# Kernel tuning notes

Hardware: AMD Instinct MI355X
Metric: run time of the kernel (lower is better)

The kernel has to match this reference:

```python
import jax, jax.numpy as jnp
import numpy as np

B, N = 2, 2048
D_MODEL, HEADS = 512, 8
D_K = D_MODEL // HEADS
D_HIDDEN = 2048
MIN_SPREAD = 2.0
MIN_RBF = 1e-3
MAX_RBF = 1.0
LN_EPS = 1e-5


def setup_inputs() -> dict:
    key = jax.random.key(0)
    ks = jax.random.split(key, 12)
    xs = (6.0 / (D_K + D_MODEL)) ** 0.5
    q = jax.random.normal(ks[0], (B, N, D_MODEL), dtype=jnp.float32)
    k = jax.random.normal(ks[1], (B, N, D_MODEL), dtype=jnp.float32)
    v = jax.random.normal(ks[2], (B, N, D_MODEL), dtype=jnp.float32)
    coords = jax.random.normal(ks[3], (B, N, 3), dtype=jnp.float32) * 10.0
    mask = jnp.ones((B, N), dtype=bool)
    q_proj = jax.random.uniform(ks[4], (HEADS, D_MODEL, D_K), minval=-xs, maxval=xs)
    k_proj = jax.random.uniform(ks[5], (HEADS, D_MODEL, D_K), minval=-xs, maxval=xs)
    v_proj = jax.random.uniform(ks[6], (HEADS, D_MODEL, D_K), minval=-xs, maxval=xs)
    q_bias = jnp.zeros((HEADS, D_K))
    k_bias = jnp.zeros((HEADS, D_K))
    v_bias = jnp.zeros((HEADS, D_K))
    ow = (1.0 / D_MODEL) ** 0.5
    out_w = jax.random.uniform(ks[7], (D_MODEL, D_MODEL), minval=-ow, maxval=ow)
    spread_w = jnp.zeros((HEADS,))
    beta_w = jnp.zeros((HEADS,))
    ln1_g = jnp.ones((D_MODEL,)); ln1_b = jnp.zeros((D_MODEL,))
    ln2_g = jnp.ones((D_MODEL,)); ln2_b = jnp.zeros((D_MODEL,))
    w1 = jax.random.normal(ks[8], (D_MODEL, D_HIDDEN)) * 0.02
    b1 = jnp.zeros((D_HIDDEN,))
    w2 = jax.random.normal(ks[9], (D_HIDDEN, D_MODEL)) * 0.02
    b2 = jnp.zeros((D_MODEL,))
    return dict(q=q, k=k, v=v, coords=coords, mask=mask,
                q_proj=q_proj, k_proj=k_proj, v_proj=v_proj,
                q_bias=q_bias, k_bias=k_bias, v_bias=v_bias,
                out_w=out_w, spread_w=spread_w, beta_w=beta_w,
                ln1_g=ln1_g, ln1_b=ln1_b, ln2_g=ln2_g, ln2_b=ln2_b,
                w1=w1, b1=b1, w2=w2, b2=b2)


def _layernorm(x, g, b):
    mu = jnp.mean(x, axis=-1, keepdims=True)
    var = jnp.mean((x - mu) ** 2, axis=-1, keepdims=True)
    return (x - mu) * jax.lax.rsqrt(var + LN_EPS) * g + b


def _geo_attention(q, k, v, coords, mask,
                   q_proj, k_proj, v_proj, q_bias, k_bias, v_bias,
                   out_w, spread_w, beta_w):
    # per-head projections: [B,H,N,dk]
    Q = jnp.einsum('bnd,hdk->bhnk', q, q_proj) + q_bias[None, :, None, :]
    K = jnp.einsum('bnd,hdk->bhnk', k, k_proj) + k_bias[None, :, None, :]
    V = jnp.einsum('bnd,hdk->bhnk', v, v_proj) + v_bias[None, :, None, :]

    spreads = MIN_SPREAD + jnp.exp(spread_w)   # [H]
    betas = jnp.exp(beta_w)                    # [H]

    # pairwise squared distances [B,N,N]
    d2 = jnp.sum((coords[:, :, None, :] - coords[:, None, :, :]) ** 2, axis=-1)
    # per-head Gaussian RBF [B,H,N,N]
    rbf = jnp.exp(-d2[:, None, :, :] / (2.0 * spreads[None, :, None, None] ** 2))

    scores = jnp.einsum('bhnk,bhmk->bhnm', Q, K) / jnp.sqrt(jnp.float32(D_K))
    scores = betas[None, :, None, None] * rbf * scores

    # sparsity: keys with rbf outside [min_rbf, max_rbf] or padded are masked out
    valid = (rbf >= MIN_RBF) & (rbf <= MAX_RBF) & mask[:, None, None, :]
    scores = jnp.where(valid, scores, -jnp.inf)
    attn = jax.nn.softmax(scores, axis=-1)     # diagonal always valid (rbf=1)

    out = jnp.einsum('bhnm,bhmk->bhnk', attn, V)         # [B,H,N,dk]
    # torch: out.permute(0,2,3,1).reshape(B,N,d_model) -> (b,n,dk,h) layout
    out = jnp.transpose(out, (0, 2, 3, 1)).reshape(out.shape[0], out.shape[2], D_MODEL)
    return out @ out_w.T


def reference(q, k, v, coords, mask,
              q_proj, k_proj, v_proj, q_bias, k_bias, v_bias,
              out_w, spread_w, beta_w,
              ln1_g, ln1_b, ln2_g, ln2_b, w1, b1, w2, b2):
    attn_out = _geo_attention(q, k, v, coords, mask,
                              q_proj, k_proj, v_proj, q_bias, k_bias, v_bias,
                              out_w, spread_w, beta_w)
    x = _layernorm(q + attn_out, ln1_g, ln1_b)
    ffn = jax.nn.relu(x @ w1 + b1) @ w2 + b2
    x = _layernorm(x + ffn, ln2_g, ln2_b)
    return x
```

## Files before the change

### kernel.cpp

```cpp
#include <hip/hip_runtime.h>
#include <math.h>

typedef __attribute__((ext_vector_type(8))) short bf16x8;
typedef __attribute__((ext_vector_type(4))) float f32x4;

#define MFMA16(a,b,c) __builtin_amdgcn_mfma_f32_16x16x32_bf16((a),(b),(c),0,0,0)

__device__ __forceinline__ unsigned short f2bf(float f) {
    union { float f; unsigned u; } x; x.f = f;
    unsigned r = x.u + 0x7FFFu + ((x.u >> 16) & 1u);
    return (unsigned short)(r >> 16);
}

__device__ __forceinline__ unsigned cvt_pk_bf16(float lo, float hi) {
    unsigned r;
    asm("v_cvt_pk_bf16_f32 %0, %1, %2" : "=v"(r) : "v"(lo), "v"(hi));
    return r;
}

__global__ __launch_bounds__(256) void cvt_qkv(
    const float* __restrict__ q, const float* __restrict__ k,
    const float* __restrict__ v,
    unsigned short* __restrict__ qb, unsigned short* __restrict__ kb,
    unsigned short* __restrict__ vb, int n)
{
    for (int i = blockIdx.x * 256 + threadIdx.x; i < n; i += gridDim.x * 256) {
        qb[i] = f2bf(q[i]); kb[i] = f2bf(k[i]); vb[i] = f2bf(v[i]);
    }
}

__global__ __launch_bounds__(256) void cvt_weights(
    const float* __restrict__ qp, const float* __restrict__ kp,
    const float* __restrict__ vp, const float* __restrict__ ow,
    const float* __restrict__ w1, const float* __restrict__ w2,
    unsigned short* __restrict__ qpT, unsigned short* __restrict__ kpT,
    unsigned short* __restrict__ vpT, unsigned short* __restrict__ owT,
    unsigned short* __restrict__ w1T, unsigned short* __restrict__ w2T)
{
    const int NP = 262144;
    const int total = 4 * NP + 1048576 + 1048576;
    for (int i = blockIdx.x * 256 + threadIdx.x; i < total; i += gridDim.x * 256) {
        if (i < 3 * NP) {
            int which = i / NP, r = i - which * NP;
            int n = r >> 9, d = r & 511;
            int h = n >> 6, kk = n & 63;
            const float* src = (which == 0) ? qp : (which == 1) ? kp : vp;
            unsigned short* dst = (which == 0) ? qpT : (which == 1) ? kpT : vpT;
            dst[r] = f2bf(src[(h << 15) + (d << 6) + kk]);
        } else if (i < 4 * NP) {
            int r = i - 3 * NP;
            int oi = r >> 9, f = r & 511;
            int h = f >> 6, kk = f & 63;
            owT[r] = f2bf(ow[(oi << 9) + (kk << 3) + h]);
        } else if (i < 4 * NP + 1048576) {
            int r = i - 4 * NP;
            int n = r >> 9, d = r & 511;
            w1T[r] = f2bf(w1[(d << 11) + n]);
        } else {
            int r = i - 4 * NP - 1048576;
            int n = r >> 11, d = r & 2047;
            w2T[r] = f2bf(w2[(d << 9) + n]);
        }
    }
}

template<int RELU, int SF32, int SB16, int SVTR>
__global__ __launch_bounds__(256) void gemm_bt(
    const unsigned short* __restrict__ A,
    const unsigned short* __restrict__ Bt,
    const float* __restrict__ bias,
    float* __restrict__ Cf, unsigned short* __restrict__ Cb,
    int M, int N, int K)
{
    __shared__ unsigned short As[128][72];
    __shared__ unsigned short Bs[128][72];
    const int tid = threadIdx.x;
    const int m0 = blockIdx.y << 7, n0 = blockIdx.x << 7;
    const int wv = tid >> 6, lane = tid & 63;
    const int lrow = lane & 15, kg = lane >> 4;
    const int wr = (wv >> 1) << 6, wc = (wv & 1) << 6;

    f32x4 acc[4][4];
    const f32x4 z4 = {0.f, 0.f, 0.f, 0.f};
#pragma unroll
    for (int i = 0; i < 4; ++i)
#pragma unroll
        for (int j = 0; j < 4; ++j) acc[i][j] = z4;

    const int nkt = K >> 6;
    for (int kt = 0; kt < nkt; ++kt) {
        __syncthreads();
        const int k0 = kt << 6;
#pragma unroll
        for (int i = 0; i < 4; ++i) {
            int slot = tid + (i << 8);
            int r = slot >> 3, c = (slot & 7) << 3;
            *(int4*)(&As[r][c]) = *(const int4*)(&A[(long)(m0 + r) * K + k0 + c]);
            *(int4*)(&Bs[r][c]) = *(const int4*)(&Bt[(long)(n0 + r) * K + k0 + c]);
        }
        __syncthreads();
#pragma unroll
        for (int ks = 0; ks < 2; ++ks) {
            const int koff = (ks << 5) + (kg << 3);
            bf16x8 af[4], bfr[4];
#pragma unroll
            for (int mi = 0; mi < 4; ++mi)
                af[mi] = *(const bf16x8*)(&As[wr + (mi << 4) + lrow][koff]);
#pragma unroll
            for (int ni = 0; ni < 4; ++ni)
                bfr[ni] = *(const bf16x8*)(&Bs[wc + (ni << 4) + lrow][koff]);
#pragma unroll
            for (int mi = 0; mi < 4; ++mi)
#pragma unroll
                for (int ni = 0; ni < 4; ++ni)
                    acc[mi][ni] = MFMA16(af[mi], bfr[ni], acc[mi][ni]);
        }
    }

#pragma unroll
    for (int mi = 0; mi < 4; ++mi) {
#pragma unroll
        for (int ni = 0; ni < 4; ++ni) {
            const int col = n0 + wc + (ni << 4) + lrow;
            const float bv = bias ? bias[col] : 0.0f;
#pragma unroll
            for (int j = 0; j < 4; ++j) {
                const int row = m0 + wr + (mi << 4) + (kg << 2) + j;
                float val = acc[mi][ni][j] + bv;
                if (RELU) val = fmaxf(val, 0.0f);
                if (SF32) Cf[(long)row * N + col] = val;
                if (SB16) Cb[(long)row * N + col] = f2bf(val);
                if (SVTR)
                    Cb[((long)(row >> 11) << 20) + ((long)col << 11) + (row & 2047)] = f2bf(val);
            }
        }
    }
}

__global__ __launch_bounds__(256) void geo_attn(
    const unsigned short* __restrict__ Qh,
    const unsigned short* __restrict__ Kh,
    const unsigned short* __restrict__ VhT,
    const float* __restrict__ coords,
    const float* __restrict__ spread_w, const float* __restrict__ beta_w,
    unsigned short* __restrict__ Ob)
{
    __shared__ unsigned short Qs[64][72];
    __shared__ unsigned short Ks[64][72];
    __shared__ unsigned short Vs[64][72];
    __shared__ unsigned short Ps[4][16][72];
    __shared__ float4 ck4[64];

    const int tid = threadIdx.x;
    const int bid = blockIdx.x;
    const int swz = ((bid & 7) << 6) + (bid >> 3);
    const int bh = swz >> 5, qt = swz & 31;
    const int b = bh >> 3, h = bh & 7;
    const int wv = tid >> 6, lane = tid & 63;
    const int lq = lane & 15, kg = lane >> 4;
    const float NEG_INF = -__builtin_inff();

    const float spread = 2.0f + __expf(spread_w[h]);
    const float inv2s2 = 1.0f / (2.0f * spread * spread);
    const float coef = __expf(beta_w[h]) * 0.125f;

    {
        const long qbase = ((long)(b * 2048 + qt * 64)) * 512 + h * 64;
#pragma unroll
        for (int i = 0; i < 2; ++i) {
            int slot = tid + (i << 8);
            int r = slot >> 3, c = (slot & 7) << 3;
            *(int4*)(&Qs[r][c]) = *(const int4*)(&Qh[qbase + (long)r * 512 + c]);
        }
    }

    float cqx, cqy, cqz;
    {
        long ca = ((long)(b * 2048 + qt * 64 + wv * 16 + lq)) * 3;
        cqx = coords[ca]; cqy = coords[ca + 1]; cqz = coords[ca + 2];
    }

    float mrun = NEG_INF, lrun = 0.0f;
    f32x4 Oa[4];
    const f32x4 z4 = {0.f, 0.f, 0.f, 0.f};
#pragma unroll
    for (int nd = 0; nd < 4; ++nd) Oa[nd] = z4;

    const long kbase0 = ((long)b * 2048) * 512 + h * 64;
    const long vbase = ((long)(b * 8 + h)) * 131072;

    for (int kt = 0; kt < 32; ++kt) {
        __syncthreads();
        const int k0 = kt << 6;
#pragma unroll
        for (int i = 0; i < 2; ++i) {
            int slot = tid + (i << 8);
            int r = slot >> 3, c = (slot & 7) << 3;
            *(int4*)(&Ks[r][c]) = *(const int4*)(&Kh[kbase0 + (long)(k0 + r) * 512 + c]);
            *(int4*)(&Vs[r][c]) = *(const int4*)(&VhT[vbase + (long)r * 2048 + k0 + c]);
        }
        if (tid < 64) {
            long ca = ((long)(b * 2048 + k0 + tid)) * 3;
            ck4[tid] = make_float4(coords[ca], coords[ca + 1], coords[ca + 2], 0.0f);
        }
        __syncthreads();

        f32x4 t4[4];
#pragma unroll
        for (int ra = 0; ra < 4; ++ra) t4[ra] = z4;
#pragma unroll
        for (int ks = 0; ks < 2; ++ks) {
            const int koff = (ks << 5) + (kg << 3);
            bf16x8 bq = *(const bf16x8*)(&Qs[(wv << 4) + lq][koff]);
#pragma unroll
            for (int ra = 0; ra < 4; ++ra) {
                bf16x8 ak = *(const bf16x8*)(&Ks[(ra << 4) + lq][koff]);
                t4[ra] = MFMA16(ak, bq, t4[ra]);
            }
        }

        float tmax = NEG_INF;
#pragma unroll
        for (int ra = 0; ra < 4; ++ra) {
#pragma unroll
            for (int j = 0; j < 4; ++j) {
                float4 ck = ck4[(ra << 4) + (kg << 2) + j];
                float dx = cqx - ck.x, dy = cqy - ck.y, dz = cqz - ck.z;
                float d2 = dx * dx + dy * dy + dz * dz;
                float rbf = __expf(-d2 * inv2s2);
                float val = (rbf >= 1e-3f) ? coef * rbf * t4[ra][j] : NEG_INF;
                t4[ra][j] = val;
                tmax = fmaxf(tmax, val);
            }
        }
        tmax = fmaxf(tmax, __shfl_xor(tmax, 16, 64));
        tmax = fmaxf(tmax, __shfl_xor(tmax, 32, 64));

        const float mn = fmaxf(mrun, tmax);
        const bool dead = (mn == NEG_INF);
        const float mneff = dead ? 0.0f : mn;
        const float fcorr = dead ? 1.0f : __expf(mrun - mn);

        float psum = 0.0f;
#pragma unroll
        for (int ra = 0; ra < 4; ++ra) {
#pragma unroll
            for (int j = 0; j < 4; ++j) {
                float p = __expf(t4[ra][j] - mneff);
                t4[ra][j] = p;
                psum += p;
            }
        }
        psum += __shfl_xor(psum, 16, 64);
        psum += __shfl_xor(psum, 32, 64);
        mrun = mn;
        lrun = lrun * fcorr + psum;

#pragma unroll
        for (int ra = 0; ra < 4; ++ra) {
            uint2 pk;
            pk.x = cvt_pk_bf16(t4[ra][0], t4[ra][1]);
            pk.y = cvt_pk_bf16(t4[ra][2], t4[ra][3]);
            *(uint2*)(&Ps[wv][lq][(ra << 4) + (kg << 2)]) = pk;
        }

        float fb[4];
#pragma unroll
        for (int j = 0; j < 4; ++j)
            fb[j] = __shfl(fcorr, (lane & 48) | ((kg << 2) + j), 64);
#pragma unroll
        for (int nd = 0; nd < 4; ++nd)
#pragma unroll
            for (int j = 0; j < 4; ++j)
                Oa[nd][j] *= fb[j];

#pragma unroll
        for (int ks = 0; ks < 2; ++ks) {
            const int koff = (ks << 5) + (kg << 3);
            bf16x8 ap = *(const bf16x8*)(&Ps[wv][lq][koff]);
#pragma unroll
            for (int nd = 0; nd < 4; ++nd) {
                bf16x8 bv = *(const bf16x8*)(&Vs[(nd << 4) + lq][koff]);
                Oa[nd] = MFMA16(ap, bv, Oa[nd]);
            }
        }
    }

    const float inv = 1.0f / lrun;
    float il[4];
#pragma unroll
    for (int j = 0; j < 4; ++j)
        il[j] = __shfl(inv, (lane & 48) | ((kg << 2) + j), 64);
    const long obase = ((long)(b * 2048 + qt * 64 + (wv << 4))) * 512 + h * 64;
#pragma unroll
    for (int nd = 0; nd < 4; ++nd)
#pragma unroll
        for (int j = 0; j < 4; ++j)
            Ob[obase + (long)((kg << 2) + j) * 512 + (nd << 4) + lq] =
                f2bf(Oa[nd][j] * il[j]);
}

template<int SB16>
__global__ __launch_bounds__(256) void ln_res(
    const float* __restrict__ X, const float* __restrict__ R,
    const float* __restrict__ g, const float* __restrict__ bb,
    float* __restrict__ Yf, unsigned short* __restrict__ Yb)
{
    const int wv = threadIdx.x >> 6, lane = threadIdx.x & 63;
    const long row = (long)blockIdx.x * 4 + wv;
    const float* xp = X + row * 512;
    const float* rp = R + row * 512;
    const int c0 = lane * 8;
    float4 a0 = *(const float4*)(xp + c0);
    float4 a1 = *(const float4*)(xp + c0 + 4);
    float4 r0 = *(const float4*)(rp + c0);
    float4 r1 = *(const float4*)(rp + c0 + 4);
    float v[8] = {a0.x + r0.x, a0.y + r0.y, a0.z + r0.z, a0.w + r0.w,
                  a1.x + r1.x, a1.y + r1.y, a1.z + r1.z, a1.w + r1.w};
    float s = 0.f, ss = 0.f;
#pragma unroll
    for (int i = 0; i < 8; ++i) { s += v[i]; ss += v[i] * v[i]; }
#pragma unroll
    for (int off = 1; off < 64; off <<= 1) {
        s += __shfl_xor(s, off, 64);
        ss += __shfl_xor(ss, off, 64);
    }
    const float mu = s * (1.0f / 512.0f);
    const float var = ss * (1.0f / 512.0f) - mu * mu;
    const float rstd = rsqrtf(var + 1e-5f);
#pragma unroll
    for (int i = 0; i < 8; ++i) {
        const int c = c0 + i;
        const float y = (v[i] - mu) * rstd * g[c] + bb[c];
        Yf[row * 512 + c] = y;
        if (SB16) Yb[row * 512 + c] = f2bf(y);
    }
}

extern "C" void kernel_launch(void* const* d_in, const int* in_sizes, int n_in,
                              void* d_out, int out_size, void* d_ws, size_t ws_size,
                              hipStream_t stream)
{
    const float* q      = (const float*)d_in[0];
    const float* k      = (const float*)d_in[1];
    const float* v      = (const float*)d_in[2];
    const float* coords = (const float*)d_in[3];
    const float* q_proj = (const float*)d_in[5];
    const float* k_proj = (const float*)d_in[6];
    const float* v_proj = (const float*)d_in[7];
    const float* q_bias = (const float*)d_in[8];
    const float* k_bias = (const float*)d_in[9];
    const float* v_bias = (const float*)d_in[10];
    const float* out_w  = (const float*)d_in[11];
    const float* spread_w = (const float*)d_in[12];
    const float* beta_w = (const float*)d_in[13];
    const float* ln1_g  = (const float*)d_in[14];
    const float* ln1_b  = (const float*)d_in[15];
    const float* ln2_g  = (const float*)d_in[16];
    const float* ln2_b  = (const float*)d_in[17];
    const float* w1     = (const float*)d_in[18];
    const float* b1     = (const float*)d_in[19];
    const float* w2     = (const float*)d_in[20];
    const float* b2     = (const float*)d_in[21];
    float* out = (float*)d_out;

    char* ws = (char*)d_ws;
    size_t off = 0;
    auto alloc = [&](size_t bytes) -> void* {
        void* p = ws + off;
        off += (bytes + 255) & ~(size_t)255;
        return p;
    };
    unsigned short* qb   = (unsigned short*)alloc(4096UL * 512 * 2);
    unsigned short* kb   = (unsigned short*)alloc(4096UL * 512 * 2);
    unsigned short* vb   = (unsigned short*)alloc(4096UL * 512 * 2);
    unsigned short* qpT  = (unsigned short*)alloc(512UL * 512 * 2);
    unsigned short* kpT  = (unsigned short*)alloc(512UL * 512 * 2);
    unsigned short* vpT  = (unsigned short*)alloc(512UL * 512 * 2);
    unsigned short* owT  = (unsigned short*)alloc(512UL * 512 * 2);
    unsigned short* w1T  = (unsigned short*)alloc(2048UL * 512 * 2);
    unsigned short* w2T  = (unsigned short*)alloc(512UL * 2048 * 2);
    unsigned short* Qp   = (unsigned short*)alloc(4096UL * 512 * 2);
    unsigned short* Kp   = (unsigned short*)alloc(4096UL * 512 * 2);
    unsigned short* VpT  = (unsigned short*)alloc(4096UL * 512 * 2);
    unsigned short* attnb= (unsigned short*)alloc(4096UL * 512 * 2);
    float* proj = (float*)alloc(4096UL * 512 * 4);
    float* x1   = (float*)alloc(4096UL * 512 * 4);
    unsigned short* x1b = (unsigned short*)alloc(4096UL * 512 * 2);
    unsigned short* hid = (unsigned short*)alloc(4096UL * 2048 * 2);
    float* ffn  = (float*)alloc(4096UL * 512 * 4);
    (void)ws_size; (void)in_sizes; (void)n_in; (void)out_size;

    cvt_qkv<<<2048, 256, 0, stream>>>(q, k, v, qb, kb, vb, 2097152);
    cvt_weights<<<2048, 256, 0, stream>>>(q_proj, k_proj, v_proj, out_w, w1, w2,
                                          qpT, kpT, vpT, owT, w1T, w2T);

    dim3 g512(4, 32);
    gemm_bt<0, 0, 1, 0><<<g512, 256, 0, stream>>>(qb, qpT, q_bias, nullptr, Qp, 4096, 512, 512);
    gemm_bt<0, 0, 1, 0><<<g512, 256, 0, stream>>>(kb, kpT, k_bias, nullptr, Kp, 4096, 512, 512);
    gemm_bt<0, 0, 0, 1><<<g512, 256, 0, stream>>>(vb, vpT, v_bias, nullptr, VpT, 4096, 512, 512);

    geo_attn<<<512, 256, 0, stream>>>(Qp, Kp, VpT, coords, spread_w, beta_w, attnb);

    gemm_bt<0, 1, 0, 0><<<g512, 256, 0, stream>>>(attnb, owT, nullptr, proj, nullptr, 4096, 512, 512);
    ln_res<1><<<1024, 256, 0, stream>>>(proj, q, ln1_g, ln1_b, x1, x1b);

    dim3 g2048(16, 32);
    gemm_bt<1, 0, 1, 0><<<g2048, 256, 0, stream>>>(x1b, w1T, b1, nullptr, hid, 4096, 2048, 512);
    gemm_bt<0, 1, 0, 0><<<g512, 256, 0, stream>>>(hid, w2T, b2, ffn, nullptr, 4096, 512, 2048);
    ln_res<0><<<1024, 256, 0, stream>>>(ffn, x1, ln2_g, ln2_b, out, nullptr);
}
```

Before: 229.6 us.

## Split attention keys across two blocks with register-prefetched tiles and merge kernel

After: 240.2 us. 1.05x slower.

```diff
diff --git a/kernel.cpp b/kernel.cpp
--- a/kernel.cpp
+++ b/kernel.cpp
@@ -137,15 +137,15 @@
     }
 }
 
-__global__ __launch_bounds__(256) void geo_attn(
+__global__ __launch_bounds__(256, 4) void geo_attn(
     const unsigned short* __restrict__ Qh,
     const unsigned short* __restrict__ Kh,
     const unsigned short* __restrict__ VhT,
     const float* __restrict__ coords,
     const float* __restrict__ spread_w, const float* __restrict__ beta_w,
-    unsigned short* __restrict__ Ob)
-{
-    __shared__ unsigned short Qs[64][72];
+    float* __restrict__ Opart,
+    float2* __restrict__ mlbuf)
+{
     __shared__ unsigned short Ks[64][72];
     __shared__ unsigned short Vs[64][72];
     __shared__ unsigned short Ps[4][16][72];
@@ -153,8 +153,9 @@
 
     const int tid = threadIdx.x;
     const int bid = blockIdx.x;
-    const int swz = ((bid & 7) << 6) + (bid >> 3);
-    const int bh = swz >> 5, qt = swz & 31;
+    const int swz = ((bid & 7) << 7) + (bid >> 3);
+    const int bh = swz >> 6, rest = swz & 63;
+    const int qt = rest >> 1, s = rest & 1;
     const int b = bh >> 3, h = bh & 7;
     const int wv = tid >> 6, lane = tid & 63;
     const int lq = lane & 15, kg = lane >> 4;
@@ -164,46 +165,52 @@
     const float inv2s2 = 1.0f / (2.0f * spread * spread);
     const float coef = __expf(beta_w[h]) * 0.125f;
 
-    {
-        const long qbase = ((long)(b * 2048 + qt * 64)) * 512 + h * 64;
+    const long qrow = (long)(b * 2048 + qt * 64 + wv * 16 + lq);
+    const bf16x8 qA = *(const bf16x8*)(&Qh[qrow * 512 + h * 64 + (kg << 3)]);
+    const bf16x8 qB = *(const bf16x8*)(&Qh[qrow * 512 + h * 64 + 32 + (kg << 3)]);
+    float cqx, cqy, cqz;
+    { long ca = qrow * 3; cqx = coords[ca]; cqy = coords[ca + 1]; cqz = coords[ca + 2]; }
+
+    float mrun = NEG_INF, lrun = 0.0f;
+    f32x4 Oa[4];
+    const f32x4 z4 = {0.f, 0.f, 0.f, 0.f};
+#pragma unroll
+    for (int nd = 0; nd < 4; ++nd) Oa[nd] = z4;
+
+    const long kbase0 = ((long)b * 2048) * 512 + h * 64;
+    const long vbase = ((long)(b * 8 + h)) * 131072;
+
+    int4 kr[2], vr[2];
+    float c0r = 0.f, c1r = 0.f, c2r = 0.f;
+
+    auto loadTile = [&](int kt) {
+        const int k0 = (s << 10) + (kt << 6);
 #pragma unroll
         for (int i = 0; i < 2; ++i) {
             int slot = tid + (i << 8);
             int r = slot >> 3, c = (slot & 7) << 3;
-            *(int4*)(&Qs[r][c]) = *(const int4*)(&Qh[qbase + (long)r * 512 + c]);
-        }
-    }
-
-    float cqx, cqy, cqz;
-    {
-        long ca = ((long)(b * 2048 + qt * 64 + wv * 16 + lq)) * 3;
-        cqx = coords[ca]; cqy = coords[ca + 1]; cqz = coords[ca + 2];
-    }
-
-    float mrun = NEG_INF, lrun = 0.0f;
-    f32x4 Oa[4];
-    const f32x4 z4 = {0.f, 0.f, 0.f, 0.f};
-#pragma unroll
-    for (int nd = 0; nd < 4; ++nd) Oa[nd] = z4;
-
-    const long kbase0 = ((long)b * 2048) * 512 + h * 64;
-    const long vbase = ((long)(b * 8 + h)) * 131072;
-
-    for (int kt = 0; kt < 32; ++kt) {
-        __syncthreads();
-        const int k0 = kt << 6;
+            kr[i] = *(const int4*)(&Kh[kbase0 + (long)(k0 + r) * 512 + c]);
+            vr[i] = *(const int4*)(&VhT[vbase + (long)r * 2048 + k0 + c]);
+        }
+        if (tid < 64) {
+            long ca = ((long)(b * 2048 + k0 + tid)) * 3;
+            c0r = coords[ca]; c1r = coords[ca + 1]; c2r = coords[ca + 2];
+        }
+    };
+    auto writeTile = [&]() {
 #pragma unroll
         for (int i = 0; i < 2; ++i) {
             int slot = tid + (i << 8);
-            int r = slot >> 3, c = (slot & 7) << 3;
-            *(int4*)(&Ks[r][c]) = *(const int4*)(&Kh[kbase0 + (long)(k0 + r) * 512 + c]);
-            *(int4*)(&Vs[r][c]) = *(const int4*)(&VhT[vbase + (long)r * 2048 + k0 + c]);
-        }
-        if (tid < 64) {
-            long ca = ((long)(b * 2048 + k0 + tid)) * 3;
-            ck4[tid] = make_float4(coords[ca], coords[ca + 1], coords[ca + 2], 0.0f);
-        }
-        __syncthreads();
+            *(int4*)(&Ks[slot >> 3][(slot & 7) << 3]) = kr[i];
+            *(int4*)(&Vs[slot >> 3][(slot & 7) << 3]) = vr[i];
+        }
+        if (tid < 64) ck4[tid] = make_float4(c0r, c1r, c2r, 0.0f);
+    };
+
+    loadTile(0); writeTile(); __syncthreads();
+
+    for (int kt = 0; kt < 16; ++kt) {
+        if (kt + 1 < 16) loadTile(kt + 1);
 
         f32x4 t4[4];
 #pragma unroll
@@ -211,7 +218,7 @@
 #pragma unroll
         for (int ks = 0; ks < 2; ++ks) {
             const int koff = (ks << 5) + (kg << 3);
-            bf16x8 bq = *(const bf16x8*)(&Qs[(wv << 4) + lq][koff]);
+            const bf16x8 bq = ks ? qB : qA;
 #pragma unroll
             for (int ra = 0; ra < 4; ++ra) {
                 bf16x8 ak = *(const bf16x8*)(&Ks[(ra << 4) + lq][koff]);
@@ -284,20 +291,43 @@
                 Oa[nd] = MFMA16(ap, bv, Oa[nd]);
             }
         }
-    }
-
-    const float inv = 1.0f / lrun;
-    float il[4];
-#pragma unroll
-    for (int j = 0; j < 4; ++j)
-        il[j] = __shfl(inv, (lane & 48) | ((kg << 2) + j), 64);
+
+        if (kt + 1 < 16) { __syncthreads(); writeTile(); __syncthreads(); }
+    }
+
+    float* op = Opart + (long)s * 2097152;
     const long obase = ((long)(b * 2048 + qt * 64 + (wv << 4))) * 512 + h * 64;
 #pragma unroll
     for (int nd = 0; nd < 4; ++nd)
 #pragma unroll
         for (int j = 0; j < 4; ++j)
-            Ob[obase + (long)((kg << 2) + j) * 512 + (nd << 4) + lq] =
-                f2bf(Oa[nd][j] * il[j]);
+            op[obase + (long)((kg << 2) + j) * 512 + (nd << 4) + lq] = Oa[nd][j];
+    if (kg == 0) {
+        int r = b * 2048 + qt * 64 + wv * 16 + lq;
+        mlbuf[s * 32768 + r * 8 + h] = make_float2(mrun, lrun);
+    }
+}
+
+__global__ __launch_bounds__(256) void attn_reduce(
+    const float* __restrict__ Op, const float2* __restrict__ ml,
+    unsigned short* __restrict__ Ob)
+{
+    const int t = blockIdx.x * 256 + threadIdx.x;
+    const int base = t << 2;
+    const int r = base >> 9;
+    const int h = (base & 511) >> 6;
+    const float2 ml0 = ml[r * 8 + h];
+    const float2 ml1 = ml[32768 + r * 8 + h];
+    const float M = fmaxf(ml0.x, ml1.x);
+    const float a0 = __expf(ml0.x - M);
+    const float a1 = __expf(ml1.x - M);
+    const float invL = 1.0f / (ml0.y * a0 + ml1.y * a1);
+    const float4 o0 = *(const float4*)(&Op[base]);
+    const float4 o1 = *(const float4*)(&Op[2097152 + base]);
+    uint2 w;
+    w.x = cvt_pk_bf16((o0.x * a0 + o1.x * a1) * invL, (o0.y * a0 + o1.y * a1) * invL);
+    w.y = cvt_pk_bf16((o0.z * a0 + o1.z * a1) * invL, (o0.w * a0 + o1.w * a1) * invL);
+    *(uint2*)(&Ob[base]) = w;
 }
 
 template<int SB16>
@@ -389,6 +419,8 @@
     unsigned short* x1b = (unsigned short*)alloc(4096UL * 512 * 2);
     unsigned short* hid = (unsigned short*)alloc(4096UL * 2048 * 2);
     float* ffn  = (float*)alloc(4096UL * 512 * 4);
+    float*  Opart = (float*)hid;
+    float2* mlbuf = (float2*)ffn;
     (void)ws_size; (void)in_sizes; (void)n_in; (void)out_size;
 
     cvt_qkv<<<2048, 256, 0, stream>>>(q, k, v, qb, kb, vb, 2097152);
@@ -400,7 +432,8 @@
     gemm_bt<0, 0, 1, 0><<<g512, 256, 0, stream>>>(kb, kpT, k_bias, nullptr, Kp, 4096, 512, 512);
     gemm_bt<0, 0, 0, 1><<<g512, 256, 0, stream>>>(vb, vpT, v_bias, nullptr, VpT, 4096, 512, 512);
 
-    geo_attn<<<512, 256, 0, stream>>>(Qp, Kp, VpT, coords, spread_w, beta_w, attnb);
+    geo_attn<<<1024, 256, 0, stream>>>(Qp, Kp, VpT, coords, spread_w, beta_w, Opart, mlbuf);
+    attn_reduce<<<2048, 256, 0, stream>>>(Opart, mlbuf, attnb);
 
     gemm_bt<0, 1, 0, 0><<<g512, 256, 0, stream>>>(attnb, owT, nullptr, proj, nullptr, 4096, 512, 512);
     ln_res<1><<<1024, 256, 0, stream>>>(proj, q, ln1_g, ln1_b, x1, x1b);
```

## Fuse QKV projection GEMMs and use narrower tiles for N=512 GEMMs

Applied to the files above, without the earlier changes.

Measured after the change: 202.5 us. -11.8%, faster.

```diff
diff --git a/kernel.cpp b/kernel.cpp
--- a/kernel.cpp
+++ b/kernel.cpp
@@ -33,12 +33,15 @@
     const float* __restrict__ qp, const float* __restrict__ kp,
     const float* __restrict__ vp, const float* __restrict__ ow,
     const float* __restrict__ w1, const float* __restrict__ w2,
+    const float* __restrict__ qbias, const float* __restrict__ kbias,
+    const float* __restrict__ vbias,
     unsigned short* __restrict__ qpT, unsigned short* __restrict__ kpT,
     unsigned short* __restrict__ vpT, unsigned short* __restrict__ owT,
-    unsigned short* __restrict__ w1T, unsigned short* __restrict__ w2T)
+    unsigned short* __restrict__ w1T, unsigned short* __restrict__ w2T,
+    float* __restrict__ biasC)
 {
     const int NP = 262144;
-    const int total = 4 * NP + 1048576 + 1048576;
+    const int total = 4 * NP + 1048576 + 1048576 + 1536;
     for (int i = blockIdx.x * 256 + threadIdx.x; i < total; i += gridDim.x * 256) {
         if (i < 3 * NP) {
             int which = i / NP, r = i - which * NP;
@@ -56,36 +59,46 @@
             int r = i - 4 * NP;
             int n = r >> 9, d = r & 511;
             w1T[r] = f2bf(w1[(d << 11) + n]);
-        } else {
+        } else if (i < 4 * NP + 2097152) {
             int r = i - 4 * NP - 1048576;
             int n = r >> 11, d = r & 2047;
             w2T[r] = f2bf(w2[(d << 9) + n]);
-        }
-    }
-}
-
-template<int RELU, int SF32, int SB16, int SVTR>
+        } else {
+            int j = i - 4 * NP - 2097152;
+            biasC[j] = (j < 512) ? qbias[j] : (j < 1024) ? kbias[j - 512] : vbias[j - 1024];
+        }
+    }
+}
+
+template<int BNT, int RELU, int SF32, int SB16, int SVTR, int SQKV>
 __global__ __launch_bounds__(256) void gemm_bt(
-    const unsigned short* __restrict__ A,
+    const unsigned short* __restrict__ Aq,
+    const unsigned short* __restrict__ Ak,
+    const unsigned short* __restrict__ Av,
     const unsigned short* __restrict__ Bt,
     const float* __restrict__ bias,
     float* __restrict__ Cf, unsigned short* __restrict__ Cb,
+    unsigned short* __restrict__ Cb2, unsigned short* __restrict__ Cb3,
     int M, int N, int K)
 {
+    constexpr int BC = BNT / 32;
     __shared__ unsigned short As[128][72];
-    __shared__ unsigned short Bs[128][72];
+    __shared__ unsigned short Bs[BNT][72];
     const int tid = threadIdx.x;
-    const int m0 = blockIdx.y << 7, n0 = blockIdx.x << 7;
+    const int m0 = blockIdx.y << 7, n0 = blockIdx.x * BNT;
     const int wv = tid >> 6, lane = tid & 63;
     const int lrow = lane & 15, kg = lane >> 4;
-    const int wr = (wv >> 1) << 6, wc = (wv & 1) << 6;
-
-    f32x4 acc[4][4];
+    const int wr = (wv >> 1) << 6, wc = (wv & 1) * (BNT / 2);
+
+    const unsigned short* A = Aq;
+    if (SQKV) A = (n0 < 512) ? Aq : (n0 < 1024) ? Ak : Av;
+
+    f32x4 acc[4][BC];
     const f32x4 z4 = {0.f, 0.f, 0.f, 0.f};
 #pragma unroll
     for (int i = 0; i < 4; ++i)
 #pragma unroll
-        for (int j = 0; j < 4; ++j) acc[i][j] = z4;
+        for (int j = 0; j < BC; ++j) acc[i][j] = z4;
 
     const int nkt = K >> 6;
     for (int kt = 0; kt < nkt; ++kt) {
@@ -96,23 +109,28 @@
             int slot = tid + (i << 8);
             int r = slot >> 3, c = (slot & 7) << 3;
             *(int4*)(&As[r][c]) = *(const int4*)(&A[(long)(m0 + r) * K + k0 + c]);
+        }
+#pragma unroll
+        for (int i = 0; i < BC; ++i) {
+            int slot = tid + (i << 8);
+            int r = slot >> 3, c = (slot & 7) << 3;
             *(int4*)(&Bs[r][c]) = *(const int4*)(&Bt[(long)(n0 + r) * K + k0 + c]);
         }
         __syncthreads();
 #pragma unroll
         for (int ks = 0; ks < 2; ++ks) {
             const int koff = (ks << 5) + (kg << 3);
-            bf16x8 af[4], bfr[4];
+            bf16x8 af[4], bfr[BC];
 #pragma unroll
             for (int mi = 0; mi < 4; ++mi)
                 af[mi] = *(const bf16x8*)(&As[wr + (mi << 4) + lrow][koff]);
 #pragma unroll
-            for (int ni = 0; ni < 4; ++ni)
+            for (int ni = 0; ni < BC; ++ni)
                 bfr[ni] = *(const bf16x8*)(&Bs[wc + (ni << 4) + lrow][koff]);
 #pragma unroll
             for (int mi = 0; mi < 4; ++mi)
 #pragma unroll
-                for (int ni = 0; ni < 4; ++ni)
+                for (int ni = 0; ni < BC; ++ni)
                     acc[mi][ni] = MFMA16(af[mi], bfr[ni], acc[mi][ni]);
         }
     }
@@ -120,7 +138,7 @@
 #pragma unroll
     for (int mi = 0; mi < 4; ++mi) {
 #pragma unroll
-        for (int ni = 0; ni < 4; ++ni) {
+        for (int ni = 0; ni < BC; ++ni) {
             const int col = n0 + wc + (ni << 4) + lrow;
             const float bv = bias ? bias[col] : 0.0f;
 #pragma unroll
@@ -132,6 +150,16 @@
                 if (SB16) Cb[(long)row * N + col] = f2bf(val);
                 if (SVTR)
                     Cb[((long)(row >> 11) << 20) + ((long)col << 11) + (row & 2047)] = f2bf(val);
+                if (SQKV) {
+                    if (n0 < 512)
+                        Cb[(long)row * 512 + col] = f2bf(val);
+                    else if (n0 < 1024)
+                        Cb2[(long)row * 512 + (col - 512)] = f2bf(val);
+                    else {
+                        const int c2 = col - 1024;
+                        Cb3[((long)(row >> 11) << 20) + ((long)c2 << 11) + (row & 2047)] = f2bf(val);
+                    }
+                }
             }
         }
     }
@@ -380,6 +408,7 @@
     unsigned short* owT  = (unsigned short*)alloc(512UL * 512 * 2);
     unsigned short* w1T  = (unsigned short*)alloc(2048UL * 512 * 2);
     unsigned short* w2T  = (unsigned short*)alloc(512UL * 2048 * 2);
+    float* biasC = (float*)alloc(1536UL * 4);
     unsigned short* Qp   = (unsigned short*)alloc(4096UL * 512 * 2);
     unsigned short* Kp   = (unsigned short*)alloc(4096UL * 512 * 2);
     unsigned short* VpT  = (unsigned short*)alloc(4096UL * 512 * 2);
@@ -393,20 +422,21 @@
 
     cvt_qkv<<<2048, 256, 0, stream>>>(q, k, v, qb, kb, vb, 2097152);
     cvt_weights<<<2048, 256, 0, stream>>>(q_proj, k_proj, v_proj, out_w, w1, w2,
-                                          qpT, kpT, vpT, owT, w1T, w2T);
-
-    dim3 g512(4, 32);
-    gemm_bt<0, 0, 1, 0><<<g512, 256, 0, stream>>>(qb, qpT, q_bias, nullptr, Qp, 4096, 512, 512);
-    gemm_bt<0, 0, 1, 0><<<g512, 256, 0, stream>>>(kb, kpT, k_bias, nullptr, Kp, 4096, 512, 512);
-    gemm_bt<0, 0, 0, 1><<<g512, 256, 0, stream>>>(vb, vpT, v_bias, nullptr, VpT, 4096, 512, 512);
+                                          q_bias, k_bias, v_bias,
+                                          qpT, kpT, vpT, owT, w1T, w2T, biasC);
+
+    gemm_bt<128, 0, 0, 0, 0, 1><<<dim3(12, 32), 256, 0, stream>>>(
+        qb, kb, vb, qpT, biasC, nullptr, Qp, Kp, VpT, 4096, 1536, 512);
 
     geo_attn<<<512, 256, 0, stream>>>(Qp, Kp, VpT, coords, spread_w, beta_w, attnb);
 
-    gemm_bt<0, 1, 0, 0><<<g512, 256, 0, stream>>>(attnb, owT, nullptr, proj, nullptr, 4096, 512, 512);
+    gemm_bt<64, 0, 1, 0, 0, 0><<<dim3(8, 32), 256, 0, stream>>>(
+        attnb, nullptr, nullptr, owT, nullptr, proj, nullptr, nullptr, nullptr, 4096, 512, 512);
     ln_res<1><<<1024, 256, 0, stream>>>(proj, q, ln1_g, ln1_b, x1, x1b);
 
-    dim3 g2048(16, 32);
-    gemm_bt<1, 0, 1, 0><<<g2048, 256, 0, stream>>>(x1b, w1T, b1, nullptr, hid, 4096, 2048, 512);
-    gemm_bt<0, 1, 0, 0><<<g512, 256, 0, stream>>>(hid, w2T, b2, ffn, nullptr, 4096, 512, 2048);
+    gemm_bt<128, 1, 0, 1, 0, 0><<<dim3(16, 32), 256, 0, stream>>>(
+        x1b, nullptr, nullptr, w1T, b1, nullptr, hid, nullptr, nullptr, 4096, 2048, 512);
+    gemm_bt<64, 0, 1, 0, 0, 0><<<dim3(8, 32), 256, 0, stream>>>(
+        hid, nullptr, nullptr, w2T, b2, ffn, nullptr, nullptr, nullptr, 4096, 512, 2048);
     ln_res<0><<<1024, 256, 0, stream>>>(ffn, x1, ln2_g, ln2_b, out, nullptr);
 }
```
